# Kernel optimization log

Hardware: AMD Instinct MI355X
Metric: run time of the kernel (lower is better)

Reference implementation:

```python
import jax, jax.numpy as jnp
import numpy as np

VOCAB, F, H1, H2 = 64, 4096, 64, 32   # vocab size, featureVectorSize, hidden dims (hard-coded 64/32/1 in source)
NBBOX, NWORDS = 8192, 16


def _uniform(key, shape, fan_in):
    # torch nn.Linear default init: U(-1/sqrt(fan_in), 1/sqrt(fan_in))
    bound = 1.0 / np.sqrt(fan_in)
    return jax.random.uniform(key, shape, jnp.float32, -bound, bound)


def setup_inputs() -> dict:
    key = jax.random.key(0)
    ks = jax.random.split(key, 8)
    x = jax.random.normal(ks[0], (NBBOX, F), jnp.float32)
    words = jax.random.randint(ks[1], (NWORDS,), 0, VOCAB)  # indices of active word-models
    # Stacked per-word MLP params (one tiny MLP per vocab word)
    W1 = _uniform(ks[2], (VOCAB, F, H1), F)
    b1 = _uniform(ks[3], (VOCAB, H1), F)
    W2 = _uniform(ks[4], (VOCAB, H1, H2), H1)
    b2 = _uniform(ks[5], (VOCAB, H2), H1)
    W3 = _uniform(ks[6], (VOCAB, H2), H2)   # Linear(32,1) weight, squeezed to [VOCAB, H2]
    b3 = _uniform(ks[7], (VOCAB,), H2)
    return {"nBBox": NBBOX, "x": x, "words": words,
            "W1": W1, "b1": b1, "W2": W2, "b2": b2, "W3": W3, "b3": b3}


def reference(nBBox, x, words, W1, b1, W2, b2, W3, b3):
    # Gather the active word-models (dict lookup in the original)
    w1, c1 = W1[words], b1[words]          # [W,F,H1], [W,H1]
    w2, c2 = W2[words], b2[words]          # [W,H1,H2], [W,H2]
    w3, c3 = W3[words], b3[words]          # [W,H2], [W]
    # Batched 3-layer MLP over all active words at once (replaces Python loop)
    h1 = jax.nn.relu(jnp.einsum('bf,wfh->wbh', x, w1) + c1[:, None, :])   # [W,B,H1]
    h2 = jax.nn.relu(jnp.einsum('wbh,whk->wbk', h1, w2) + c2[:, None, :])  # [W,B,H2]
    logits = jnp.einsum('wbk,wk->wb', h2, w3) + c3[:, None]                # [W,B]
    # output = ones(nBBox,1) * prod_w sigmoid(logits_w)
    return jnp.prod(jax.nn.sigmoid(logits), axis=0)[:, None]               # [B,1]
```

## Files before the change

### kernel.cpp

```cpp
#include <hip/hip_runtime.h>
#include <stdint.h>
#include <math.h>

#define NBBOX 8192
#define FDIM  4096
#define H1DIM 64
#define H2DIM 32
#define NW    16
#define NCOL  1024

typedef __attribute__((ext_vector_type(8))) _Float16 f16x8;
typedef __attribute__((ext_vector_type(4))) float    f32x4;

typedef __attribute__((address_space(1))) void* gptr_t;
typedef __attribute__((address_space(3))) void* lptr_t;

__device__ __forceinline__ void g2l16(const void* g, void* l) {
    __builtin_amdgcn_global_load_lds((gptr_t)(uintptr_t)g,
                                     (lptr_t)(uint32_t)(uintptr_t)l,
                                     16, 0, 0);
}

__global__ void convert_x(const float* __restrict__ x, _Float16* __restrict__ xh) {
    int gid = blockIdx.x * blockDim.x + threadIdx.x;
    int idx = gid * 8;
    float4 a = *(const float4*)(x + idx);
    float4 b = *(const float4*)(x + idx + 4);
    f16x8 h;
    h[0] = (_Float16)a.x; h[1] = (_Float16)a.y; h[2] = (_Float16)a.z; h[3] = (_Float16)a.w;
    h[4] = (_Float16)b.x; h[5] = (_Float16)b.y; h[6] = (_Float16)b.z; h[7] = (_Float16)b.w;
    *(f16x8*)(xh + idx) = h;
}

__global__ __launch_bounds__(256) void gather_w(
    const float* __restrict__ W1, const int* __restrict__ words,
    uint32_t* __restrict__ bth_u32)
{
    __shared__ uint32_t t[64 * 69];
    const int wi = blockIdx.x >> 5;
    const int ft = blockIdx.x & 31;
    const int f0 = ft * 128;
    const int w  = words[wi];
    const int tid  = threadIdx.x;
    const int c    = tid & 63;
    const int fgrp = tid >> 6;

    const float* src = W1 + ((size_t)w * FDIM + f0) * H1DIM + c;
#pragma unroll
    for (int p = 0; p < 16; ++p) {
        const int f = fgrp * 2 + p * 8;
        float v0 = src[(size_t)f * H1DIM];
        float v1 = src[(size_t)(f + 1) * H1DIM];
        union { _Float16 h[2]; uint32_t u; } pk;
        pk.h[0] = (_Float16)v0; pk.h[1] = (_Float16)v1;
        t[c * 69 + (f >> 1)] = pk.u;
    }
    __syncthreads();
#pragma unroll
    for (int p = 0; p < 16; ++p) {
        const int cc = p * 4 + (tid >> 6);
        const int fd = tid & 63;
        bth_u32[(size_t)(wi * 64 + cc) * (FDIM / 2) + ft * 64 + fd] = t[cc * 69 + fd];
    }
}

__global__ __launch_bounds__(256, 2) void gemm_l1(
    const _Float16* __restrict__ xh, const _Float16* __restrict__ bth,
    const float* __restrict__ b1, const int* __restrict__ words,
    float* __restrict__ Hout)
{
    __shared__ _Float16 As[2][128 * 32];
    __shared__ _Float16 Bs[2][128 * 32];

    const int mt   = blockIdx.x >> 3;
    const int nt   = blockIdx.x & 7;
    const int t    = threadIdx.x;
    const int w    = t >> 6;
    const int lane = t & 63;
    const int m0 = mt * 128, n0 = nt * 128;

    f32x4 acc[4][4] = {};

    const int rs = w * 16 + (lane >> 2);
    const int kc = (lane & 3) * 8;

    const _Float16* A = xh  + (size_t)m0 * FDIM;
    const _Float16* B = bth + (size_t)n0 * FDIM;

    const int wm = w >> 1, wn = w & 1;
    const int ml = lane & 15;
    const int q8 = (lane >> 4) * 8;

    for (int kt = 0; kt < 64; ++kt) {
        const int k0 = kt * 64;
#pragma unroll
        for (int s = 0; s < 2; ++s) {
            const int kp = k0 + s * 32 + kc;
            g2l16(A + (size_t)rs * FDIM + kp,        &As[s][w * 512]);
            g2l16(A + (size_t)(rs + 64) * FDIM + kp, &As[s][2048 + w * 512]);
            g2l16(B + (size_t)rs * FDIM + kp,        &Bs[s][w * 512]);
            g2l16(B + (size_t)(rs + 64) * FDIM + kp, &Bs[s][2048 + w * 512]);
        }
        __syncthreads();

#pragma unroll
        for (int s = 0; s < 2; ++s) {
            f16x8 af[4], bfr[4];
#pragma unroll
            for (int i = 0; i < 4; ++i)
                af[i] = *(const f16x8*)&As[s][(wm * 64 + i * 16 + ml) * 32 + q8];
#pragma unroll
            for (int j = 0; j < 4; ++j)
                bfr[j] = *(const f16x8*)&Bs[s][(wn * 64 + j * 16 + ml) * 32 + q8];
#pragma unroll
            for (int i = 0; i < 4; ++i)
#pragma unroll
                for (int j = 0; j < 4; ++j)
                    acc[i][j] = __builtin_amdgcn_mfma_f32_16x16x32_f16(af[i], bfr[j], acc[i][j], 0, 0, 0);
        }
        __syncthreads();
    }

    const int q = lane >> 4;
#pragma unroll
    for (int j = 0; j < 4; ++j) {
        const int gcol = n0 + wn * 64 + j * 16 + ml;
        const float bias = b1[words[gcol >> 6] * H1DIM + (gcol & 63)];
#pragma unroll
        for (int i = 0; i < 4; ++i) {
            const int grow0 = m0 + wm * 64 + i * 16 + q * 4;
#pragma unroll
            for (int r = 0; r < 4; ++r) {
                float v = acc[i][j][r] + bias;
                Hout[(size_t)(grow0 + r) * NCOL + gcol] = v > 0.f ? v : 0.f;
            }
        }
    }
}

__global__ __launch_bounds__(256) void tail_mlp(
    const float* __restrict__ Hbuf, const int* __restrict__ words,
    const float* __restrict__ W2, const float* __restrict__ b2,
    const float* __restrict__ W3, const float* __restrict__ b3,
    float* __restrict__ sig)
{
    __shared__ float tile[4][64 * 64];
    const int t    = threadIdx.x;
    const int v    = t >> 6;
    const int lane = t & 63;
    const int wi   = blockIdx.x >> 5;
    const int rb   = blockIdx.x & 31;
    const int r0   = rb * 256 + v * 64;
    const int wv   = words[wi];

    {
        const int rr = lane >> 4;
        const int kch = lane & 15;
#pragma unroll
        for (int p = 0; p < 16; ++p) {
            const int row = p * 4 + rr;
            float4 d = *(const float4*)&Hbuf[(size_t)(r0 + row) * NCOL + wi * H1DIM + kch * 4];
            const int pos = ((kch + row) & 7) | (kch & 8);
            *(float4*)&tile[v][row * 64 + pos * 4] = d;
        }
    }

    const float* W2w = W2 + (size_t)wv * (H1DIM * H2DIM);
    float acc[H2DIM];
#pragma unroll
    for (int j = 0; j < H2DIM; ++j) acc[j] = 0.f;

#pragma unroll
    for (int c = 0; c < 16; ++c) {
        const int pos = ((c + lane) & 7) | (c & 8);
        f32x4 h = *(const f32x4*)&tile[v][lane * 64 + pos * 4];
#pragma unroll
        for (int kk = 0; kk < 4; ++kk) {
            const float hv = h[kk];
            const int k = c * 4 + kk;
#pragma unroll
            for (int j = 0; j < H2DIM; ++j)
                acc[j] = fmaf(hv, W2w[k * H2DIM + j], acc[j]);
        }
    }

    float logit = b3[wv];
#pragma unroll
    for (int j = 0; j < H2DIM; ++j) {
        float h2 = acc[j] + b2[wv * H2DIM + j];
        h2 = h2 > 0.f ? h2 : 0.f;
        logit = fmaf(h2, W3[wv * H2DIM + j], logit);
    }
    sig[(size_t)wi * NBBOX + r0 + lane] = 1.f / (1.f + expf(-logit));
}

__global__ void prod_k(const float* __restrict__ sig, float* __restrict__ out) {
    const int r = blockIdx.x * 256 + threadIdx.x;
    float p = 1.f;
#pragma unroll
    for (int wi = 0; wi < NW; ++wi) p *= sig[(size_t)wi * NBBOX + r];
    out[r] = p;
}

extern "C" void kernel_launch(void* const* d_in, const int* in_sizes, int n_in,
                              void* d_out, int out_size, void* d_ws, size_t ws_size,
                              hipStream_t stream)
{
    const float* x   = (const float*)d_in[1];
    const int* words = (const int*)  d_in[2];
    const float* W1  = (const float*)d_in[3];
    const float* b1  = (const float*)d_in[4];
    const float* W2  = (const float*)d_in[5];
    const float* b2  = (const float*)d_in[6];
    const float* W3  = (const float*)d_in[7];
    const float* b3  = (const float*)d_in[8];
    float* out = (float*)d_out;

    char* ws = (char*)d_ws;
    _Float16* xh  = (_Float16*)(ws);
    _Float16* bth = (_Float16*)(ws + 67108864);
    float*    Hb  = (float*)   (ws + 67108864 + 8388608);
    float*    sig = (float*)   (ws);

    convert_x<<<NBBOX * FDIM / 8 / 256, 256, 0, stream>>>(x, xh);
    gather_w<<<512, 256, 0, stream>>>(W1, words, (uint32_t*)bth);
    gemm_l1<<<512, 256, 0, stream>>>(xh, bth, b1, words, Hb);
    tail_mlp<<<512, 256, 0, stream>>>(Hb, words, W2, b2, W3, b3, sig);
    prod_k<<<NBBOX / 256, 256, 0, stream>>>(sig, out);
}
```

Before: 343.9 us.

## Fuse tail MLP into GEMM epilogue and merge prep kernels

The layer-2/3 MLP and sigmoid now run inside the layer-1 GEMM epilogue. Each wave stages its 64x64 ReLU tile in a 64KB shared buffer that reuses the GEMM staging memory, so the 32MB hidden-activation buffer is never written to or read back from global memory. The fp16 conversion of x and the W1 gather/transposition are merged into one launch. Block indexing is reordered so consecutive blocks share the same weight tile. In exchange, GEMM blocks use more shared memory and registers in the epilogue, which may lower occupancy.

```diff
diff --git a/kernel.cpp b/kernel.cpp
--- a/kernel.cpp
+++ b/kernel.cpp
@@ -21,27 +21,30 @@
                                      16, 0, 0);
 }
 
-__global__ void convert_x(const float* __restrict__ x, _Float16* __restrict__ xh) {
-    int gid = blockIdx.x * blockDim.x + threadIdx.x;
-    int idx = gid * 8;
-    float4 a = *(const float4*)(x + idx);
-    float4 b = *(const float4*)(x + idx + 4);
-    f16x8 h;
-    h[0] = (_Float16)a.x; h[1] = (_Float16)a.y; h[2] = (_Float16)a.z; h[3] = (_Float16)a.w;
-    h[4] = (_Float16)b.x; h[5] = (_Float16)b.y; h[6] = (_Float16)b.z; h[7] = (_Float16)b.w;
-    *(f16x8*)(xh + idx) = h;
-}
-
-__global__ __launch_bounds__(256) void gather_w(
+__global__ __launch_bounds__(256) void prep(
+    const float* __restrict__ x, _Float16* __restrict__ xh,
     const float* __restrict__ W1, const int* __restrict__ words,
     uint32_t* __restrict__ bth_u32)
 {
     __shared__ uint32_t t[64 * 69];
+    const int tid = threadIdx.x;
+
+    if (blockIdx.x >= 512) {
+        const int gid = (blockIdx.x - 512) * 256 + tid;
+        const int idx = gid * 8;
+        float4 a = *(const float4*)(x + idx);
+        float4 b = *(const float4*)(x + idx + 4);
+        f16x8 h;
+        h[0] = (_Float16)a.x; h[1] = (_Float16)a.y; h[2] = (_Float16)a.z; h[3] = (_Float16)a.w;
+        h[4] = (_Float16)b.x; h[5] = (_Float16)b.y; h[6] = (_Float16)b.z; h[7] = (_Float16)b.w;
+        *(f16x8*)(xh + idx) = h;
+        return;
+    }
+
     const int wi = blockIdx.x >> 5;
     const int ft = blockIdx.x & 31;
     const int f0 = ft * 128;
     const int w  = words[wi];
-    const int tid  = threadIdx.x;
     const int c    = tid & 63;
     const int fgrp = tid >> 6;
 
@@ -64,16 +67,20 @@
     }
 }
 
-__global__ __launch_bounds__(256, 2) void gemm_l1(
+__global__ __launch_bounds__(256, 2) void gemm_fused(
     const _Float16* __restrict__ xh, const _Float16* __restrict__ bth,
     const float* __restrict__ b1, const int* __restrict__ words,
-    float* __restrict__ Hout)
+    const float* __restrict__ W2, const float* __restrict__ b2,
+    const float* __restrict__ W3, const float* __restrict__ b3,
+    float* __restrict__ sig)
 {
-    __shared__ _Float16 As[2][128 * 32];
-    __shared__ _Float16 Bs[2][128 * 32];
-
-    const int mt   = blockIdx.x >> 3;
-    const int nt   = blockIdx.x & 7;
+    __shared__ __align__(16) char smem[65536];
+    _Float16 (*As)[128 * 32] = (_Float16 (*)[128 * 32])smem;
+    _Float16 (*Bs)[128 * 32] = (_Float16 (*)[128 * 32])(smem + 16384);
+    float* tile = (float*)smem;
+
+    const int mt   = blockIdx.x & 63;
+    const int nt   = blockIdx.x >> 6;
     const int t    = threadIdx.x;
     const int w    = t >> 6;
     const int lane = t & 63;
@@ -121,77 +128,55 @@
         __syncthreads();
     }
 
-    const int q = lane >> 4;
+    const int q  = lane >> 4;
+    const int wi = nt * 2 + wn;
+    const int wv = __builtin_amdgcn_readfirstlane(words[wi]);
+    float* tw = tile + w * 4096;
+
 #pragma unroll
     for (int j = 0; j < 4; ++j) {
-        const int gcol = n0 + wn * 64 + j * 16 + ml;
-        const float bias = b1[words[gcol >> 6] * H1DIM + (gcol & 63)];
+        const int col = j * 16 + ml;
+        const float bias = b1[wv * H1DIM + col];
+        const int c = col >> 2, e = col & 3;
 #pragma unroll
         for (int i = 0; i < 4; ++i) {
-            const int grow0 = m0 + wm * 64 + i * 16 + q * 4;
 #pragma unroll
             for (int r = 0; r < 4; ++r) {
+                const int row = i * 16 + q * 4 + r;
+                const int pos = ((c + row) & 7) | (c & 8);
                 float v = acc[i][j][r] + bias;
-                Hout[(size_t)(grow0 + r) * NCOL + gcol] = v > 0.f ? v : 0.f;
+                tw[row * 64 + pos * 4 + e] = v > 0.f ? v : 0.f;
             }
         }
     }
-}
-
-__global__ __launch_bounds__(256) void tail_mlp(
-    const float* __restrict__ Hbuf, const int* __restrict__ words,
-    const float* __restrict__ W2, const float* __restrict__ b2,
-    const float* __restrict__ W3, const float* __restrict__ b3,
-    float* __restrict__ sig)
-{
-    __shared__ float tile[4][64 * 64];
-    const int t    = threadIdx.x;
-    const int v    = t >> 6;
-    const int lane = t & 63;
-    const int wi   = blockIdx.x >> 5;
-    const int rb   = blockIdx.x & 31;
-    const int r0   = rb * 256 + v * 64;
-    const int wv   = words[wi];
-
-    {
-        const int rr = lane >> 4;
-        const int kch = lane & 15;
-#pragma unroll
-        for (int p = 0; p < 16; ++p) {
-            const int row = p * 4 + rr;
-            float4 d = *(const float4*)&Hbuf[(size_t)(r0 + row) * NCOL + wi * H1DIM + kch * 4];
-            const int pos = ((kch + row) & 7) | (kch & 8);
-            *(float4*)&tile[v][row * 64 + pos * 4] = d;
-        }
-    }
 
     const float* W2w = W2 + (size_t)wv * (H1DIM * H2DIM);
-    float acc[H2DIM];
-#pragma unroll
-    for (int j = 0; j < H2DIM; ++j) acc[j] = 0.f;
-
-#pragma unroll
-    for (int c = 0; c < 16; ++c) {
-        const int pos = ((c + lane) & 7) | (c & 8);
-        f32x4 h = *(const f32x4*)&tile[v][lane * 64 + pos * 4];
+    float a2[H2DIM];
+#pragma unroll
+    for (int j = 0; j < H2DIM; ++j) a2[j] = 0.f;
+
+#pragma unroll
+    for (int c2 = 0; c2 < 16; ++c2) {
+        const int pos = ((c2 + lane) & 7) | (c2 & 8);
+        f32x4 h = *(const f32x4*)&tw[lane * 64 + pos * 4];
 #pragma unroll
         for (int kk = 0; kk < 4; ++kk) {
             const float hv = h[kk];
-            const int k = c * 4 + kk;
+            const int k = c2 * 4 + kk;
 #pragma unroll
             for (int j = 0; j < H2DIM; ++j)
-                acc[j] = fmaf(hv, W2w[k * H2DIM + j], acc[j]);
+                a2[j] = fmaf(hv, W2w[k * H2DIM + j], a2[j]);
         }
     }
 
     float logit = b3[wv];
 #pragma unroll
     for (int j = 0; j < H2DIM; ++j) {
-        float h2 = acc[j] + b2[wv * H2DIM + j];
+        float h2 = a2[j] + b2[wv * H2DIM + j];
         h2 = h2 > 0.f ? h2 : 0.f;
         logit = fmaf(h2, W3[wv * H2DIM + j], logit);
     }
-    sig[(size_t)wi * NBBOX + r0 + lane] = 1.f / (1.f + expf(-logit));
+    sig[(size_t)wi * NBBOX + m0 + wm * 64 + lane] = 1.f / (1.f + expf(-logit));
 }
 
 __global__ void prod_k(const float* __restrict__ sig, float* __restrict__ out) {
@@ -219,12 +204,9 @@
     char* ws = (char*)d_ws;
     _Float16* xh  = (_Float16*)(ws);
     _Float16* bth = (_Float16*)(ws + 67108864);
-    float*    Hb  = (float*)   (ws + 67108864 + 8388608);
-    float*    sig = (float*)   (ws);
-
-    convert_x<<<NBBOX * FDIM / 8 / 256, 256, 0, stream>>>(x, xh);
-    gather_w<<<512, 256, 0, stream>>>(W1, words, (uint32_t*)bth);
-    gemm_l1<<<512, 256, 0, stream>>>(xh, bth, b1, words, Hb);
-    tail_mlp<<<512, 256, 0, stream>>>(Hb, words, W2, b2, W3, b3, sig);
+    float*    sig = (float*)   (ws + 67108864 + 8388608);
+
+    prep<<<512 + NBBOX * FDIM / 8 / 256, 256, 0, stream>>>(x, xh, W1, words, (uint32_t*)bth);
+    gemm_fused<<<512, 256, 0, stream>>>(xh, bth, b1, words, W2, b2, W3, b3, sig);
     prod_k<<<NBBOX / 256, 256, 0, stream>>>(sig, out);
 }
```

Result: faster. 327.4 us (-4.8%).
